# Kernel tuning notes

Measured on AMD Instinct MI355X. Metric: run time of the kernel, lower is better.

The kernel has to match this reference:

```python
import jax, jax.numpy as jnp
import numpy as np

B, NQ, NK, D = 8, 2048, 2048, 1024

def setup_inputs() -> dict:
    key = jax.random.key(0)
    k1, k2, k3, k4, k5 = jax.random.split(key, 5)
    query_input = jax.random.normal(k1, (B, NQ, D), dtype=jnp.float32)
    key_input = jax.random.normal(k2, (B, NK, D), dtype=jnp.float32)
    s = 1.0 / np.sqrt(D)
    # nn.Linear(in,out,bias=False): y = x @ W.T, W shape (out,in)
    Wq = jax.random.uniform(k3, (D, D), dtype=jnp.float32, minval=-s, maxval=s)
    Wk = jax.random.uniform(k4, (D, D), dtype=jnp.float32, minval=-s, maxval=s)
    Wv = jax.random.uniform(k5, (D, D), dtype=jnp.float32, minval=-s, maxval=s)
    return {"query_input": query_input, "key_input": key_input,
            "Wq": Wq, "Wk": Wk, "Wv": Wv}

def reference(query_input, key_input, Wq, Wk, Wv):
    d = query_input.shape[-1]
    q = jnp.einsum('bnd,ed->bne', query_input, Wq)   # (b, n_q, d)
    k = jnp.einsum('bmd,ed->bme', key_input, Wk)     # (b, n_k, d)
    v = jnp.einsum('bnd,ed->bne', query_input, Wv)   # (b, n_q, d) -- value from query_input
    # scores: K @ Q^T -> (b, n_k, n_q), softmax over n_q
    a = jnp.einsum('bmd,bnd->bmn', k, q) / jnp.sqrt(jnp.float32(d))
    a = jax.nn.softmax(a, axis=-1)
    context = jnp.einsum('bmn,bnd->bmd', a, v)       # (b, n_k, d)
    return context + key_input
```

## Files before the change

### kernel.cpp

```cpp
#include <hip/hip_runtime.h>
#include <hip/hip_bf16.h>

using bf16 = __bf16;
typedef __bf16 bf16x8 __attribute__((ext_vector_type(8)));
typedef float f32x4 __attribute__((ext_vector_type(4)));

__device__ __forceinline__ void gload_lds16(const bf16* g, bf16* l) {
  __builtin_amdgcn_global_load_lds(
      (const __attribute__((address_space(1))) void*)g,
      (__attribute__((address_space(3))) void*)l, 16, 0, 0);
}

__global__ __launch_bounds__(256) void cvt_f32_bf16(const float* __restrict__ in,
                                                    bf16* __restrict__ out, int n) {
  int i = (blockIdx.x * 256 + threadIdx.x) * 8;
  if (i >= n) return;
  float4 f0 = *(const float4*)&in[i];
  float4 f1 = *(const float4*)&in[i + 4];
  bf16x8 o;
  o[0] = (bf16)f0.x; o[1] = (bf16)f0.y; o[2] = (bf16)f0.z; o[3] = (bf16)f0.w;
  o[4] = (bf16)f1.x; o[5] = (bf16)f1.y; o[6] = (bf16)f1.z; o[7] = (bf16)f1.w;
  *(bf16x8*)&out[i] = o;
}

__device__ __forceinline__ void load_frags(const bf16* __restrict__ buf,
                                           int wr, int wc, int lk, int lr,
                                           bf16x8 (&R)[12]) {
#pragma unroll
  for (int mi = 0; mi < 8; ++mi) {
    const int r = wr * 128 + mi * 16 + lr;
    R[mi] = *(const bf16x8*)&buf[r * 32 + ((lk ^ ((r >> 1) & 3)) << 3)];
  }
#pragma unroll
  for (int ni = 0; ni < 4; ++ni) {
    const int r = wc * 64 + ni * 16 + lr;
    R[8 + ni] = *(const bf16x8*)&buf[8192 + r * 32 + ((lk ^ ((r >> 1) & 3)) << 3)];
  }
}

__device__ __forceinline__ void mfma_tile(const bf16x8 (&R)[12], f32x4 (&acc)[8][4]) {
  __builtin_amdgcn_s_setprio(1);
#pragma unroll
  for (int mi = 0; mi < 8; ++mi)
#pragma unroll
    for (int ni = 0; ni < 4; ++ni)
      acc[mi][ni] = __builtin_amdgcn_mfma_f32_16x16x32_bf16(R[mi], R[8 + ni], acc[mi][ni], 0, 0, 0);
  __builtin_amdgcn_s_setprio(0);
}

template <int EPI>
__global__ __launch_bounds__(512, 2)
void gemm_bt(const bf16* __restrict__ A, const bf16* __restrict__ B,
             void* __restrict__ Cv, const float* __restrict__ Add,
             const float* __restrict__ Inv,
             int K, int lda, int ldb, int ldc,
             long sA, long sB, long sC, long sAdd, float scale) {
  int bx = blockIdx.x, by = blockIdx.y, bz = blockIdx.z;
  if (gridDim.z > 1) {
    const int gx = gridDim.x, gxy = gx * gridDim.y;
    const int nwg = gxy * gridDim.z;
    int lin = bx + gx * by + gxy * bz;
    lin = (lin & 7) * (nwg >> 3) + (lin >> 3);
    bz = lin / gxy; const int rem = lin - bz * gxy;
    by = rem / gx;  bx = rem - by * gx;
  }
  A += (long)bz * sA;
  B += (long)bz * sB;
  const int tid = threadIdx.x;
  const int lane = tid & 63;
  const int wave = tid >> 6;
  const int wr = wave >> 2;
  const int wc = wave & 3;
  const long brow = (long)bx * 256;
  const long bcol = (long)by * 256;

  __shared__ bf16 lds[4][16384];

  f32x4 acc[8][4] = {};

  const int srow = tid >> 2;
  const int scg  = (tid & 3) ^ ((srow >> 1) & 3);
  const bf16* gA = A + (brow + srow) * (long)lda + scg * 8;
  const bf16* gB = B + (bcol + srow) * (long)ldb + scg * 8;
  const long a128 = (long)lda << 7;
  const long b128 = (long)ldb << 7;

  const int nk = K >> 5;

  auto stage = [&](int t) {
    bf16* buf = (bf16*)lds[t & 3];
    const bf16* a = gA + (long)t * 32;
    const bf16* b = gB + (long)t * 32;
    gload_lds16(a,        buf + tid * 8);
    gload_lds16(a + a128, buf + 4096 + tid * 8);
    gload_lds16(b,        buf + 8192 + tid * 8);
    gload_lds16(b + b128, buf + 12288 + tid * 8);
  };

  const int lk = lane >> 4;
  const int lr = lane & 15;

  stage(0); stage(1); stage(2);
  asm volatile("s_waitcnt vmcnt(4)" ::: "memory");
  __builtin_amdgcn_s_barrier();

  bf16x8 R0[12], R1[12];
  load_frags((const bf16*)lds[0], wr, wc, lk, lr, R0);

  for (int t = 0; t < nk; t += 2) {
    load_frags((const bf16*)lds[(t + 1) & 3], wr, wc, lk, lr, R1);
    if (t + 3 < nk) stage(t + 3);
    mfma_tile(R0, acc);
    if (t + 3 < nk) { asm volatile("s_waitcnt vmcnt(4)" ::: "memory"); }
    else            { asm volatile("s_waitcnt vmcnt(0)" ::: "memory"); }
    __builtin_amdgcn_s_barrier();
    if (t + 2 < nk) load_frags((const bf16*)lds[(t + 2) & 3], wr, wc, lk, lr, R0);
    if (t + 4 < nk) stage(t + 4);
    mfma_tile(R1, acc);
    if (t + 4 < nk) { asm volatile("s_waitcnt vmcnt(4)" ::: "memory"); }
    else            { asm volatile("s_waitcnt vmcnt(0)" ::: "memory"); }
    __builtin_amdgcn_s_barrier();
  }

  const int or0 = wr * 128 + ((lane >> 4) << 2);
  const int oc0 = wc * 64 + (lane & 15);
#pragma unroll
  for (int mi = 0; mi < 8; ++mi) {
#pragma unroll
    for (int ni = 0; ni < 4; ++ni) {
#pragma unroll
      for (int j = 0; j < 4; ++j) {
        const long row = brow + or0 + mi * 16 + j;
        const long col = bcol + oc0 + ni * 16;
        if constexpr (EPI == 0) {
          bf16* C = (bf16*)Cv + (long)bz * sC;
          C[row * ldc + col] = (bf16)(acc[mi][ni][j] * scale);
        } else if constexpr (EPI == 1) {
          bf16* C = (bf16*)Cv + (long)bz * sC;
          C[row * ldc + col] = (bf16)__expf(acc[mi][ni][j] * scale);
        } else {
          float* C = (float*)Cv + (long)bz * sC;
          const float* Ad = Add + (long)bz * sAdd;
          const float* iv = Inv + (long)bz * 2048;
          C[row * ldc + col] = acc[mi][ni][j] * iv[row] + Ad[row * ldc + col];
        }
      }
    }
  }
}

__global__ __launch_bounds__(256) void rowsum_inv(const bf16* __restrict__ E,
                                                  float* __restrict__ inv) {
  const long row = blockIdx.x;
  const bf16* p = E + row * 2048;
  const int tid = threadIdx.x;
  bf16x8 v = *(const bf16x8*)&p[tid * 8];
  float s = 0.f;
#pragma unroll
  for (int i = 0; i < 8; ++i) s += (float)v[i];
#pragma unroll
  for (int off = 32; off > 0; off >>= 1) s += __shfl_xor(s, off, 64);
  __shared__ float red[4];
  if ((tid & 63) == 0) red[tid >> 6] = s;
  __syncthreads();
  if (tid == 0) inv[row] = 1.0f / (red[0] + red[1] + red[2] + red[3]);
}

extern "C" void kernel_launch(void* const* d_in, const int* in_sizes, int n_in,
                              void* d_out, int out_size, void* d_ws, size_t ws_size,
                              hipStream_t stream) {
  const float* q_in = (const float*)d_in[0];
  const float* k_in = (const float*)d_in[1];
  const float* Wq   = (const float*)d_in[2];
  const float* Wk   = (const float*)d_in[3];
  const float* Wv   = (const float*)d_in[4];
  float* out = (float*)d_out;
  char* ws = (char*)d_ws;

  bf16* qb  = (bf16*)(ws);
  bf16* kb  = (bf16*)(ws + 33554432);
  bf16* S   = (bf16*)(ws);
  bf16* Wqb = (bf16*)(ws + 67108864);
  float* inv = (float*)(ws + 67108864);
  bf16* Wkb = (bf16*)(ws + 69206016);
  bf16* Wvb = (bf16*)(ws + 71303168);
  bf16* Qp  = (bf16*)(ws + 73400320);
  bf16* Kp  = (bf16*)(ws + 106954752);
  bf16* Vpt = (bf16*)(ws + 140509184);

  cvt_f32_bf16<<<8192, 256, 0, stream>>>(q_in, qb, 16777216);
  cvt_f32_bf16<<<8192, 256, 0, stream>>>(k_in, kb, 16777216);
  cvt_f32_bf16<<<512, 256, 0, stream>>>(Wq, Wqb, 1048576);
  cvt_f32_bf16<<<512, 256, 0, stream>>>(Wk, Wkb, 1048576);
  cvt_f32_bf16<<<512, 256, 0, stream>>>(Wv, Wvb, 1048576);

  gemm_bt<0><<<dim3(64, 4, 1), 512, 0, stream>>>(
      qb, Wqb, Qp, nullptr, nullptr, 1024, 1024, 1024, 1024, 0, 0, 0, 0, 1.0f);
  gemm_bt<0><<<dim3(64, 4, 1), 512, 0, stream>>>(
      kb, Wkb, Kp, nullptr, nullptr, 1024, 1024, 1024, 1024, 0, 0, 0, 0, 1.0f);
  gemm_bt<0><<<dim3(4, 8, 8), 512, 0, stream>>>(
      Wvb, qb, Vpt, nullptr, nullptr, 1024, 1024, 1024, 2048,
      0L, 2097152L, 2097152L, 0L, 1.0f);

  gemm_bt<1><<<dim3(8, 8, 8), 512, 0, stream>>>(
      Kp, Qp, S, nullptr, nullptr, 1024, 1024, 1024, 2048,
      2097152L, 2097152L, 4194304L, 0L, 0.03125f);

  rowsum_inv<<<16384, 256, 0, stream>>>(S, inv);

  gemm_bt<2><<<dim3(8, 4, 8), 512, 0, stream>>>(
      S, Vpt, out, k_in, inv, 2048, 2048, 2048, 1024,
      4194304L, 2097152L, 2097152L, 2097152L, 1.0f);
}
```

Baseline: 315.9 us.

## Fold Wq and Wk into one precomputed matrix to drop a projection GEMM

The scores are reassociated as k_in·(Wk^T·Wq)·q_in^T. The small 1024x1024 product G is computed once with a split-K atomic GEMM on transposed bf16 weights. The large key-projection GEMM then becomes kb·G, and the query projection is removed entirely because the score GEMM uses the bf16 query input directly. The final epilogue also reads the residual from the bf16 copy of key_input instead of the fp32 original, which cuts epilogue traffic but adds bf16 rounding error to the output. G is also rounded to bf16, which changes the accumulation error of the scores.

```diff
diff --git a/kernel.cpp b/kernel.cpp
--- a/kernel.cpp
+++ b/kernel.cpp
@@ -23,6 +23,95 @@
   *(bf16x8*)&out[i] = o;
 }
 
+__global__ __launch_bounds__(256) void tcvt_f32_bf16(const float* __restrict__ in,
+                                                     bf16* __restrict__ out,
+                                                     int R, int C) {
+  __shared__ float tile[64][65];
+  const int t = threadIdx.x;
+  const int r0 = blockIdx.y * 64, c0 = blockIdx.x * 64;
+  const int r = t >> 4, c4 = (t & 15) * 4;
+#pragma unroll
+  for (int rr = 0; rr < 64; rr += 16) {
+    float4 v = *(const float4*)&in[(long)(r0 + r + rr) * C + c0 + c4];
+    tile[r + rr][c4 + 0] = v.x; tile[r + rr][c4 + 1] = v.y;
+    tile[r + rr][c4 + 2] = v.z; tile[r + rr][c4 + 3] = v.w;
+  }
+  __syncthreads();
+  const int cc = t >> 2, rseg = (t & 3) * 16;
+  bf16 tmp[16];
+#pragma unroll
+  for (int k = 0; k < 16; ++k) tmp[k] = (bf16)tile[rseg + k][cc];
+  *(bf16x8*)&out[(long)(c0 + cc) * R + r0 + rseg] = *(bf16x8*)&tmp[0];
+  *(bf16x8*)&out[(long)(c0 + cc) * R + r0 + rseg + 8] = *(bf16x8*)&tmp[8];
+}
+
+__global__ __launch_bounds__(256) void zero_f32(float* __restrict__ p, int n) {
+  int i = (blockIdx.x * 256 + threadIdx.x) * 4;
+  if (i < n) *(float4*)&p[i] = make_float4(0.f, 0.f, 0.f, 0.f);
+}
+
+__global__ __launch_bounds__(256)
+void gemm_small_atomic(const bf16* __restrict__ A, const bf16* __restrict__ B,
+                       float* __restrict__ C, int lda, int ldb, int ldc) {
+  const int tid = threadIdx.x;
+  const int wave = tid >> 6;
+  const int lane = tid & 63;
+  const int wr = wave >> 1, wc = wave & 1;
+  const long brow = (long)blockIdx.x * 128;
+  const long bcol = (long)blockIdx.y * 128;
+  const int kofs = blockIdx.z * 256;
+
+  __shared__ bf16 As[128 * 32];
+  __shared__ bf16 Bs[128 * 32];
+  f32x4 acc[4][4] = {};
+
+  const int r0 = tid >> 2;
+  const int c0 = (tid & 3) * 8;
+  const bf16* ga = A + (brow + r0) * (long)lda + kofs + c0;
+  const bf16* gb = B + (bcol + r0) * (long)ldb + kofs + c0;
+  bf16* la0 = As + tid * 8;
+  bf16* la1 = As + 2048 + tid * 8;
+  bf16* lb0 = Bs + tid * 8;
+  bf16* lb1 = Bs + 2048 + tid * 8;
+  const int afo = (wr * 64 + (lane & 15)) * 32 + (lane >> 4) * 8;
+  const int bfo = (wc * 64 + (lane & 15)) * 32 + (lane >> 4) * 8;
+
+  for (int kt = 0; kt < 8; ++kt) {
+    gload_lds16(ga, la0);
+    gload_lds16(ga + (long)64 * lda, la1);
+    gload_lds16(gb, lb0);
+    gload_lds16(gb + (long)64 * ldb, lb1);
+    ga += 32; gb += 32;
+    __syncthreads();
+    bf16x8 av[4], bv[4];
+#pragma unroll
+    for (int i = 0; i < 4; ++i) {
+      av[i] = *(const bf16x8*)&As[afo + i * 512];
+      bv[i] = *(const bf16x8*)&Bs[bfo + i * 512];
+    }
+#pragma unroll
+    for (int mi = 0; mi < 4; ++mi)
+#pragma unroll
+      for (int ni = 0; ni < 4; ++ni)
+        acc[mi][ni] = __builtin_amdgcn_mfma_f32_16x16x32_bf16(av[mi], bv[ni],
+                                                              acc[mi][ni], 0, 0, 0);
+    __syncthreads();
+  }
+
+  const int or0 = wr * 64 + ((lane >> 4) << 2);
+  const int oc0 = wc * 64 + (lane & 15);
+#pragma unroll
+  for (int mi = 0; mi < 4; ++mi)
+#pragma unroll
+    for (int ni = 0; ni < 4; ++ni)
+#pragma unroll
+      for (int j = 0; j < 4; ++j) {
+        const long row = brow + or0 + mi * 16 + j;
+        const long col = bcol + oc0 + ni * 16;
+        atomicAdd(&C[row * ldc + col], acc[mi][ni][j]);
+      }
+}
+
 __device__ __forceinline__ void load_frags(const bf16* __restrict__ buf,
                                            int wr, int wc, int lk, int lr,
                                            bf16x8 (&R)[12]) {
@@ -51,7 +140,7 @@
 template <int EPI>
 __global__ __launch_bounds__(512, 2)
 void gemm_bt(const bf16* __restrict__ A, const bf16* __restrict__ B,
-             void* __restrict__ Cv, const float* __restrict__ Add,
+             void* __restrict__ Cv, const bf16* __restrict__ Add,
              const float* __restrict__ Inv,
              int K, int lda, int ldb, int ldc,
              long sA, long sB, long sC, long sAdd, float scale) {
@@ -140,9 +229,9 @@
           C[row * ldc + col] = (bf16)__expf(acc[mi][ni][j] * scale);
         } else {
           float* C = (float*)Cv + (long)bz * sC;
-          const float* Ad = Add + (long)bz * sAdd;
+          const bf16* Ad = Add + (long)bz * sAdd;
           const float* iv = Inv + (long)bz * 2048;
-          C[row * ldc + col] = acc[mi][ni][j] * iv[row] + Ad[row * ldc + col];
+          C[row * ldc + col] = acc[mi][ni][j] * iv[row] + (float)Ad[row * ldc + col];
         }
       }
     }
@@ -177,38 +266,42 @@
   float* out = (float*)d_out;
   char* ws = (char*)d_ws;
 
-  bf16* qb  = (bf16*)(ws);
-  bf16* kb  = (bf16*)(ws + 33554432);
-  bf16* S   = (bf16*)(ws);
-  bf16* Wqb = (bf16*)(ws + 67108864);
-  float* inv = (float*)(ws + 67108864);
-  bf16* Wkb = (bf16*)(ws + 69206016);
-  bf16* Wvb = (bf16*)(ws + 71303168);
-  bf16* Qp  = (bf16*)(ws + 73400320);
-  bf16* Kp  = (bf16*)(ws + 106954752);
-  bf16* Vpt = (bf16*)(ws + 140509184);
-
+  bf16*  qb   = (bf16*)(ws);
+  bf16*  kb   = (bf16*)(ws + 33554432);
+  bf16*  S    = (bf16*)(ws + 67108864);
+  float* GTf  = (float*)(ws + 67108864);
+  bf16*  GTb  = (bf16*)(ws + 71303168);
+  bf16*  T1   = (bf16*)(ws + 134217728);
+  bf16*  Vpt  = (bf16*)(ws + 134217728);
+  bf16*  Wvb  = (bf16*)(ws + 167772160);
+  bf16*  WqTb = (bf16*)(ws + 169869312);
+  bf16*  WkTb = (bf16*)(ws + 171966464);
+  float* inv  = (float*)(ws + 169869312);
+
+  zero_f32<<<1024, 256, 0, stream>>>(GTf, 1048576);
+  tcvt_f32_bf16<<<dim3(16, 16), 256, 0, stream>>>(Wq, WqTb, 1024, 1024);
+  tcvt_f32_bf16<<<dim3(16, 16), 256, 0, stream>>>(Wk, WkTb, 1024, 1024);
   cvt_f32_bf16<<<8192, 256, 0, stream>>>(q_in, qb, 16777216);
   cvt_f32_bf16<<<8192, 256, 0, stream>>>(k_in, kb, 16777216);
-  cvt_f32_bf16<<<512, 256, 0, stream>>>(Wq, Wqb, 1048576);
-  cvt_f32_bf16<<<512, 256, 0, stream>>>(Wk, Wkb, 1048576);
   cvt_f32_bf16<<<512, 256, 0, stream>>>(Wv, Wvb, 1048576);
 
+  gemm_small_atomic<<<dim3(8, 8, 4), 256, 0, stream>>>(WqTb, WkTb, GTf, 1024, 1024, 1024);
+  cvt_f32_bf16<<<512, 256, 0, stream>>>(GTf, GTb, 1048576);
+
   gemm_bt<0><<<dim3(64, 4, 1), 512, 0, stream>>>(
-      qb, Wqb, Qp, nullptr, nullptr, 1024, 1024, 1024, 1024, 0, 0, 0, 0, 1.0f);
-  gemm_bt<0><<<dim3(64, 4, 1), 512, 0, stream>>>(
-      kb, Wkb, Kp, nullptr, nullptr, 1024, 1024, 1024, 1024, 0, 0, 0, 0, 1.0f);
+      kb, GTb, T1, nullptr, nullptr, 1024, 1024, 1024, 1024, 0, 0, 0, 0, 1.0f);
+
+  gemm_bt<1><<<dim3(8, 8, 8), 512, 0, stream>>>(
+      T1, qb, S, nullptr, nullptr, 1024, 1024, 1024, 2048,
+      2097152L, 2097152L, 4194304L, 0L, 0.03125f);
+
   gemm_bt<0><<<dim3(4, 8, 8), 512, 0, stream>>>(
       Wvb, qb, Vpt, nullptr, nullptr, 1024, 1024, 1024, 2048,
       0L, 2097152L, 2097152L, 0L, 1.0f);
 
-  gemm_bt<1><<<dim3(8, 8, 8), 512, 0, stream>>>(
-      Kp, Qp, S, nullptr, nullptr, 1024, 1024, 1024, 2048,
-      2097152L, 2097152L, 4194304L, 0L, 0.03125f);
-
   rowsum_inv<<<16384, 256, 0, stream>>>(S, inv);
 
   gemm_bt<2><<<dim3(8, 4, 8), 512, 0, stream>>>(
-      S, Vpt, out, k_in, inv, 2048, 2048, 2048, 1024,
+      S, Vpt, out, kb, inv, 2048, 2048, 2048, 1024,
       4194304L, 2097152L, 2097152L, 2097152L, 1.0f);
 }
```

Result: faster. 298.6 us (-5.5%).
